# Kernel tuning notes

Measured on AMD Instinct MI355X. Metric: run time of the kernel, lower is better.

## Reference

```python
import jax, jax.numpy as jnp
import numpy as np

B, L, E, H, V, ENC = 64, 51, 512, 512, 30000, 2048


def setup_inputs() -> dict:
    key = jax.random.key(0)
    ks = jax.random.split(key, 12)
    encoder_out = jax.random.normal(ks[0], (B, ENC), jnp.float32)
    encoded_captions = jax.random.randint(ks[1], (B, L), 0, V)
    lengths = jax.random.randint(ks[2], (B,), 2, L + 1)
    lengths = lengths.at[0].set(L)  # ensure max(decode_lengths) == L-1 so T is static
    caption_lengths = lengths[:, None]

    def lin(k, out_d, in_d):
        bnd = 1.0 / np.sqrt(in_d)
        kw, kb = jax.random.split(k)
        w = jax.random.uniform(kw, (out_d, in_d), jnp.float32, -bnd, bnd)
        b = jax.random.uniform(kb, (out_d,), jnp.float32, -bnd, bnd)
        return w, b

    embedding_weight = jax.random.uniform(ks[3], (V, E), jnp.float32, -0.1, 0.1)
    w_ih, b_ih = lin(ks[4], 4 * H, E)
    w_hh, b_hh = lin(ks[5], 4 * H, H)
    w_init_h, b_init_h = lin(ks[6], H, ENC)
    w_init_c, b_init_c = lin(ks[7], H, ENC)
    w_fc = jax.random.uniform(ks[8], (V, H), jnp.float32, -0.1, 0.1)
    b_fc = jnp.zeros((V,), jnp.float32)
    return dict(encoder_out=encoder_out, encoded_captions=encoded_captions,
                caption_lengths=caption_lengths, embedding_weight=embedding_weight,
                w_ih=w_ih, b_ih=b_ih, w_hh=w_hh, b_hh=b_hh,
                w_init_h=w_init_h, b_init_h=b_init_h,
                w_init_c=w_init_c, b_init_c=b_init_c, w_fc=w_fc, b_fc=b_fc)


def _forward(encoder_out, embedding_weight, w_ih, b_ih, w_hh, b_hh,
             w_init_h, b_init_h, w_init_c, b_init_c, w_fc, b_fc,
             encoded_captions, caption_lengths):
    lengths = caption_lengths[:, 0]
    sort_ind = jnp.argsort(-lengths)          # descending-length sort
    enc = encoder_out[sort_ind]
    caps = encoded_captions[sort_ind]
    dec_len = lengths[sort_ind] - 1           # [B]
    embs = embedding_weight[caps]             # [B, L, E]
    h0 = enc @ w_init_h.T + b_init_h          # [B, H]
    c0 = enc @ w_init_c.T + b_init_c
    T = caps.shape[1] - 1                     # static max(decode_lengths)
    xs = (jnp.transpose(embs[:, :T], (1, 0, 2)), jnp.arange(T))

    # Note: the torch loop trims h,c to batch_size_t; because lengths are
    # sorted descending, trimmed rows never produce outputs again, so running
    # the full batch and masking finished rows yields identical predictions.
    def step(carry, xt):
        h, c = carry
        x, t = xt
        gates = x @ w_ih.T + b_ih + h @ w_hh.T + b_hh   # [B, 4H]
        i, f, g, o = jnp.split(gates, 4, axis=-1)       # LSTMCell gate order
        c = jax.nn.sigmoid(f) * c + jax.nn.sigmoid(i) * jnp.tanh(g)
        h = jax.nn.sigmoid(o) * jnp.tanh(c)
        preds = h @ w_fc.T + b_fc                        # dropout = identity (eval)
        preds = jnp.where((t < dec_len)[:, None], preds, 0.0)
        return (h, c), preds

    _, preds = jax.lax.scan(step, (h0, c0), xs)          # [T, B, V]
    predictions = jnp.transpose(preds, (1, 0, 2))        # [B, T, V]
    return predictions, caps, dec_len, sort_ind


def reference(encoder_out, encoded_captions, caption_lengths, embedding_weight,
              w_ih, b_ih, w_hh, b_hh, w_init_h, b_init_h, w_init_c, b_init_c,
              w_fc, b_fc):
    return _forward(encoder_out, embedding_weight, w_ih, b_ih, w_hh, b_hh,
                    w_init_h, b_init_h, w_init_c, b_init_c, w_fc, b_fc,
                    encoded_captions, caption_lengths)
```

## Files before the change

kernel.cpp:

```cpp
#include <hip/hip_runtime.h>

#define NB    64
#define LCAP  51
#define TT    50
#define HID   512
#define EMB   512
#define VOC   30000
#define ENCD  2048
#define G4    2048

typedef unsigned short u16;
typedef unsigned int   u32;
typedef __attribute__((ext_vector_type(8))) short bf16x8;
typedef __attribute__((ext_vector_type(4))) float f32x4;
typedef __attribute__((ext_vector_type(4))) unsigned int u32x4;

__device__ __forceinline__ u16 f2bf(float x) {
  union { float f; unsigned u; } v; v.f = x;
  unsigned r = v.u + 0x7fffu + ((v.u >> 16) & 1u);
  return (u16)(r >> 16);
}

__device__ __forceinline__ float fast_sigmoid(float x) {
  return 1.f / (1.f + __expf(-x));
}
__device__ __forceinline__ float fast_tanh(float x) {
  float xx = fminf(fmaxf(x, -10.f), 10.f);
  float e = __expf(2.f * xx);
  return (e - 1.f) * __frcp_rn(e + 1.f);
}

template <int SLEEP>
__device__ __forceinline__ void poll_flags16(const int* flg, int lane, u32 tt) {
  if (lane < 16) {
    const u32* myp = (const u32*)flg + lane;
    u32 f;
    for (;;) {
      asm volatile("global_load_dword %0, %1, off sc0 sc1"
                   : "=v"(f) : "v"(myp) : "memory");
      asm volatile("s_waitcnt vmcnt(0)" : "+v"(f) :: "memory");
      if (((f & 0xffu) >= tt) & (((f >> 8) & 0xffu) >= tt) &
          (((f >> 16) & 0xffu) >= tt) & ((f >> 24) >= tt)) break;
      __builtin_amdgcn_s_sleep(SLEEP);
    }
  }
}

__global__ __launch_bounds__(256) void sort_k(const int* __restrict__ cap_len,
                                              const int* __restrict__ caps,
                                              float* __restrict__ out,
                                              int* __restrict__ sind,
                                              int* __restrict__ dlen,
                                              int* __restrict__ trow,
                                              int* __restrict__ zmap,
                                              int* __restrict__ nact,
                                              int* __restrict__ flags,
                                              int* __restrict__ tileneed) {
  __shared__ int smlen[NB];
  __shared__ int smpos[NB];
  __shared__ int sdl[NB];
  __shared__ int cnt_s[TT];
  __shared__ int toff_s[TT];
  __shared__ int trow_s[NB * TT];
  int tid = threadIdx.x;
  if (tid < NB) { smlen[tid] = cap_len[tid]; flags[tid] = 0; }
  __syncthreads();
  if (tid < NB) {
    int li = smlen[tid];
    int rank = 0;
    for (int j = 0; j < NB; ++j) {
      int lj = smlen[j];
      rank += (lj > li || (lj == li && j < tid)) ? 1 : 0;
    }
    smpos[rank] = tid;
  }
  __syncthreads();
  if (tid < NB) {
    int src = smpos[tid];
    int dl = smlen[src] - 1;
    sind[tid] = src;
    dlen[tid] = dl;
    sdl[tid] = dl;
    float* caps_out = out + (size_t)NB * TT * VOC;
    for (int l = 0; l < LCAP; ++l)
      caps_out[tid * LCAP + l] = (float)caps[src * LCAP + l];
    out[96003264 + tid] = (float)dl;
    out[96003328 + tid] = (float)src;
  }
  __syncthreads();
  if (tid < TT) {
    int c = 0;
    for (int b = 0; b < NB; ++b) c += (sdl[b] > tid) ? 1 : 0;
    cnt_s[tid] = c;
  }
  __syncthreads();
  if (tid == 0) {
    int s = 0;
    for (int t = 0; t < TT; ++t) { toff_s[t] = s; s += cnt_s[t]; }
    *nact = s;
  }
  __syncthreads();
  if (tid < TT) {
    int t = tid;
    int o = toff_s[t];
    int z = t * NB - o;
    int c = cnt_s[t];
    for (int b = 0; b < NB; ++b) {
      int m = b * TT + t;
      if (b < c) trow_s[o + b] = m;
      else       zmap[z + (b - c)] = m;
    }
  }
  __syncthreads();
  int na = toff_s[TT - 1] + cnt_s[TT - 1];
  for (int k = tid; k < na; k += 256) trow[k] = trow_s[k];
  if (tid < 25) {
    int i = tid;
    if (i * 128 < na) {
      int k = min(i * 128 + 127, na - 1);
      tileneed[i] = (trow_s[k] % TT) + 2;
    }
  }
}

__global__ __launch_bounds__(256) void prep_k(const float* __restrict__ w_ih,
                                              const float* __restrict__ wh,
                                              const float* __restrict__ wc,
                                              const float* __restrict__ enc,
                                              const float* __restrict__ emb,
                                              const float* __restrict__ w_fc,
                                              const int* __restrict__ caps,
                                              const int* __restrict__ sind,
                                              u16* __restrict__ Wih,
                                              u16* __restrict__ Winit,
                                              u16* __restrict__ Ebf,
                                              u16* __restrict__ Xb,
                                              u16* __restrict__ Wfc) {
  int i = blockIdx.x * 256 + threadIdx.x;
  const float* src;
  u16* dstp;
  if (i < 262144) {
    src = w_ih + (size_t)i * 4;
    dstp = Wih + (size_t)i * 4;
  } else if (i < 786432) {
    int e = (i - 262144) * 4;
    int row = e >> 11, col = e & 2047;
    src = (row < 512) ? (wh + (size_t)row * 2048 + col)
                      : (wc + (size_t)(row - 512) * 2048 + col);
    dstp = Winit + (size_t)(i - 262144) * 4;
  } else if (i < 819200) {
    int e = (i - 786432) * 4;
    int r = e >> 11, k = e & 2047;
    src = enc + (size_t)sind[r] * ENCD + k;
    dstp = Ebf + (size_t)(i - 786432) * 4;
  } else if (i < 1228800) {
    int e = (i - 819200) * 4;
    int m = e >> 9, k = e & 511;
    unsigned b = ((unsigned)m * 5243u) >> 18;
    int t = m - (int)b * TT;
    int cap = caps[sind[b] * LCAP + t];
    src = emb + (size_t)cap * EMB + k;
    dstp = Xb + (size_t)(i - 819200) * 4;
  } else if (i < 5068800) {
    size_t idx = (size_t)(i - 1228800) * 4;
    src = w_fc + idx;
    dstp = Wfc + idx;
  } else return;
  float4 v = *(const float4*)src;
  ushort4 o;
  o.x = f2bf(v.x); o.y = f2bf(v.y); o.z = f2bf(v.z); o.w = f2bf(v.w);
  *(ushort4*)dstp = o;
}

#define BM 128
#define BN 128
#define BK 32
#define LDT 40

template <int EPI>
__global__ __launch_bounds__(256) void gemm_bt(const u16* __restrict__ A,
                                               const u16* __restrict__ Bm,
                                               int Mr, int Nr, int K,
                                               void* __restrict__ outv,
                                               float* __restrict__ out1,
                                               const float* __restrict__ bias0,
                                               const float* __restrict__ bias1) {
  __shared__ u16 As[BM * LDT];
  __shared__ u16 Bs[BN * LDT];
  int tid = threadIdx.x;
  int mBase = blockIdx.x * BM;
  int nBase = blockIdx.y * BN;

  int wid = tid >> 6, lane = tid & 63;
  int wm = (wid >> 1) * 64, wn = (wid & 1) * 64;
  int lm = lane & 15, lq = lane >> 4;

  f32x4 acc[4][4];
  for (int i = 0; i < 4; ++i)
    for (int j = 0; j < 4; ++j)
      acc[i][j] = (f32x4){0.f, 0.f, 0.f, 0.f};

  int nkt = K / BK;
  for (int kt = 0; kt < nkt; ++kt) {
    for (int it = 0; it < 2; ++it) {
      int li = tid + it * 256;
      int row = li >> 2, kq = li & 3;
      {
        int gr = min(mBase + row, Mr - 1);
        uint4 v = *(const uint4*)(A + (size_t)gr * K + kt * BK + kq * 8);
        *(uint4*)&As[row * LDT + kq * 8] = v;
      }
      {
        int gr = min(nBase + row, Nr - 1);
        uint4 v = *(const uint4*)(Bm + (size_t)gr * K + kt * BK + kq * 8);
        *(uint4*)&Bs[row * LDT + kq * 8] = v;
      }
    }
    __syncthreads();
    bf16x8 af[4], bfr[4];
    for (int i = 0; i < 4; ++i)
      af[i] = *(const bf16x8*)&As[(wm + i * 16 + lm) * LDT + lq * 8];
    for (int j = 0; j < 4; ++j)
      bfr[j] = *(const bf16x8*)&Bs[(wn + j * 16 + lm) * LDT + lq * 8];
    for (int i = 0; i < 4; ++i)
      for (int j = 0; j < 4; ++j)
        acc[i][j] = __builtin_amdgcn_mfma_f32_16x16x32_bf16(af[i], bfr[j], acc[i][j], 0, 0, 0);
    __syncthreads();
  }

  for (int i = 0; i < 4; ++i) {
    int rloc0 = wm + i * 16 + (lane >> 4) * 4;
    for (int j = 0; j < 4; ++j) {
      int col = nBase + wn + j * 16 + (lane & 15);
      for (int r = 0; r < 4; ++r) {
        int rloc = rloc0 + r;
        float v = acc[i][j][r];
        if (EPI == 0) {
          int row = mBase + rloc;
          if (row < Mr && col < Nr)
            ((float*)outv)[(size_t)row * Nr + col] = v + bias0[col] + bias1[col];
        } else {
          int row = mBase + rloc;
          if (row < Mr && col < Nr) {
            if (col < 512) {
              int jj = col >> 3;
              ((u16*)outv)[(size_t)jj * 512 + row * 8 + (col & 7)] = f2bf(v + bias0[col]);
            } else {
              out1[(size_t)row * 512 + (col - 512)] = v + bias1[col - 512];
            }
          }
        }
      }
    }
  }
}

__global__ __launch_bounds__(256, 1) void lstm_fc(const float* __restrict__ w_hh,
                                                  const float* __restrict__ xW,
                                                  const float* __restrict__ cbuf,
                                                  u32* __restrict__ hx,
                                                  u32* __restrict__ Hs32,
                                                  int* __restrict__ flg,
                                                  const u16* __restrict__ Wfc,
                                                  const float* __restrict__ b_fc,
                                                  const int* __restrict__ trow,
                                                  const int* __restrict__ zmap,
                                                  const int* __restrict__ nactp,
                                                  const int* __restrict__ tileneed,
                                                  float* __restrict__ out) {
  __shared__ __align__(16) char smem[43520];
  int tid = threadIdx.x;
  int wave = tid >> 6, lane = tid & 63;
  int lm = lane & 15, lq = lane >> 4;

  if (blockIdx.x < 64) {
    u16* wsm = (u16*)smem;
    float* gsmf = (float*)(smem + 33280);
    u32* hsh = (u32*)(smem + 33280 + 9216);
#define GSM(rr, cc) gsmf[(rr) * 36 + (cc)]
    int j = blockIdx.x;
    int u0 = j * 8;

    {
      int r = tid >> 3;
      int cc = (tid & 7) * 64;
      const float* src = w_hh + (size_t)((r >> 3) * HID + u0 + (r & 7)) * HID + cc;
      u16* dst = &wsm[r * 520 + cc];
#pragma unroll
      for (int q = 0; q < 16; ++q) {
        float4 v = ((const float4*)src)[q];
        ushort4 o; o.x = f2bf(v.x); o.y = f2bf(v.y); o.z = f2bf(v.z); o.w = f2bf(v.w);
        ((ushort4*)dst)[q] = o;
      }
    }
    __syncthreads();

    bf16x8 bfrag[2][16];
#pragma unroll
    for (int n = 0; n < 2; ++n)
#pragma unroll
      for (int kq = 0; kq < 16; ++kq)
        bfrag[n][kq] = *(const bf16x8*)&wsm[(n * 16 + lm) * 520 + kq * 32 + lq * 8];

    int b = tid >> 2, up = tid & 3;
    float creg[2];
    {
      float2 c2 = *(const float2*)&cbuf[(size_t)b * HID + u0 + 2 * up];
      creg[0] = c2.x; creg[1] = c2.y;
    }

    const int abase = lq * 256 + (wave * 16 + lm) * 4;

    for (int t = 0; t < TT; ++t) {
      const u32* hcur = hx + (size_t)(t & 1) * (NB * 256);
      u32* hnxt = hx + (size_t)((t + 1) & 1) * (NB * 256);

      float xg[4][2];
      {
        const float* xwp = xW + (size_t)(b * TT + t) * G4 + u0 + 2 * up;
#pragma unroll
        for (int g = 0; g < 4; ++g) {
          float2 v = *(const float2*)&xwp[g * HID];
          xg[g][0] = v.x; xg[g][1] = v.y;
        }
      }

      if (t > 0) {
        if (wave == 0) poll_flags16<1>(flg, lane, (u32)t);
        __syncthreads();
      }

      u32x4 raw[16];
#pragma unroll
      for (int kq = 0; kq < 16; ++kq) {
        const u32* p = hcur + abase + kq * 1024;
        asm volatile("global_load_dwordx4 %0, %1, off sc0 sc1"
                     : "=v"(raw[kq]) : "v"(p) : "memory");
      }
      asm volatile("s_waitcnt vmcnt(0)"
                   : "+v"(raw[0]), "+v"(raw[1]), "+v"(raw[2]), "+v"(raw[3]),
                     "+v"(raw[4]), "+v"(raw[5]), "+v"(raw[6]), "+v"(raw[7]),
                     "+v"(raw[8]), "+v"(raw[9]), "+v"(raw[10]), "+v"(raw[11]),
                     "+v"(raw[12]), "+v"(raw[13]), "+v"(raw[14]), "+v"(raw[15])
                   :: "memory");

      f32x4 acc0 = (f32x4){0.f, 0.f, 0.f, 0.f};
      f32x4 acc1 = (f32x4){0.f, 0.f, 0.f, 0.f};
#pragma unroll
      for (int kq = 0; kq < 16; ++kq) {
        bf16x8 a = __builtin_bit_cast(bf16x8, raw[kq]);
        acc0 = __builtin_amdgcn_mfma_f32_16x16x32_bf16(a, bfrag[0][kq], acc0, 0, 0, 0);
        acc1 = __builtin_amdgcn_mfma_f32_16x16x32_bf16(a, bfrag[1][kq], acc1, 0, 0, 0);
      }
#pragma unroll
      for (int r = 0; r < 4; ++r) {
        GSM(wave * 16 + lq * 4 + r, lm)      = acc0[r];
        GSM(wave * 16 + lq * 4 + r, 16 + lm) = acc1[r];
      }

      float hn2[2];
#pragma unroll
      for (int e = 0; e < 2; ++e) {
        int ul = 2 * up + e;
        float gi = GSM(b, ul)      + xg[0][e];
        float gf = GSM(b, 8 + ul)  + xg[1][e];
        float gg = GSM(b, 16 + ul) + xg[2][e];
        float go = GSM(b, 24 + ul) + xg[3][e];
        float cn = fast_sigmoid(gf) * creg[e] + fast_sigmoid(gi) * fast_tanh(gg);
        creg[e] = cn;
        hn2[e] = fast_sigmoid(go) * fast_tanh(cn);
      }
      hsh[b * 4 + up] = (u32)f2bf(hn2[0]) | ((u32)f2bf(hn2[1]) << 16);
      __syncthreads();

      if (tid < 64) {
        u32x4 hv = *(const u32x4*)&hsh[tid * 4];
        u32* dst = hnxt + j * 256 + tid * 4;
        asm volatile("global_store_dwordx4 %0, %1, off sc0 sc1"
                     :: "v"(dst), "v"(hv) : "memory");
        asm volatile("s_waitcnt vmcnt(0)" ::: "memory");
        if (tid == 0) {
          u32 fv = (u32)(t + 1);
          unsigned char* fj = (unsigned char*)flg + j;
          asm volatile("global_store_byte %0, %1, off sc0 sc1"
                       :: "v"(fj), "v"(fv) : "memory");
        }
        u32* hdst = Hs32 + (size_t)t * 16384 + j * 256 + tid * 4;
        asm volatile("global_store_dwordx4 %0, %1, off sc0 sc1"
                     :: "v"(hdst), "v"(hv) : "memory");
      }
    }
    if (wave == 0) {
      asm volatile("s_waitcnt vmcnt(0)" ::: "memory");
      if (lane == 0) {
        u32 fv = 51u;
        unsigned char* fj = (unsigned char*)flg + j;
        asm volatile("global_store_byte %0, %1, off sc0 sc1"
                     :: "v"(fj), "v"(fv) : "memory");
      }
    }
#undef GSM
  } else {
    u16* As = (u16*)smem;
    u16* Bs = (u16*)(smem + 10240);
    int* rmap_s = (int*)(smem + 20480);
    int* hsl_s = (int*)(smem + 20992);
    int* tn_s = (int*)(smem + 21504);
    const u16* HsU = (const u16*)Hs32;

    if (tid < 25) tn_s[tid] = tileneed[tid];
    int nactv = nactp[0];
    int ntiles = (nactv + 127) >> 7;
    int totjobs = ntiles * 235;
    __syncthreads();

    const int F = 192;
    int f = blockIdx.x - 64;
    int fs = (f & 7) * 24 + (f >> 3);
    int per = (totjobs + F - 1) / F;
    int J0 = fs * per;
    int J1 = min(J0 + per, totjobs);
    int wm = (wave >> 1) * 64, wn = (wave & 1) * 64;

    if (J0 < J1) {
      int p0 = J0 / ntiles, p1 = (J1 - 1) / ntiles;

      int lastNeed = 0;
      for (int rt = 0; rt < ntiles; ++rt) {
        int need = tn_s[rt];
        bool any = false;
        for (int p = p0; p <= p1; ++p) {
          int J = p * ntiles + rt;
          if (J >= J0 && J < J1) { any = true; break; }
        }
        if (!any) continue;
        if (need > lastNeed) {
          if (wave == 0) poll_flags16<64>(flg, lane, (u32)need);
          lastNeed = need;
        }
        __syncthreads();
        if (tid < 128) {
          int k = (rt << 7) + tid;
          int m = trow[(k < nactv) ? k : (nactv - 1)];
          int bb = (m * 5243) >> 18;
          int tt = m - bb * TT;
          rmap_s[tid] = m;
          hsl_s[tid] = tt * 32768 + bb * 8;
        }
        __syncthreads();

        for (int p = p0; p <= p1; ++p) {
          int J = p * ntiles + rt;
          if (J < J0 || J >= J1) continue;
          int nBase = p * 128;

          f32x4 acc[4][4];
          for (int i = 0; i < 4; ++i)
            for (int jj = 0; jj < 4; ++jj)
              acc[i][jj] = (f32x4){0.f, 0.f, 0.f, 0.f};

          for (int kt = 0; kt < 16; ++kt) {
            for (int it = 0; it < 2; ++it) {
              int li = tid + it * 256;
              int row = li >> 2, kq = li & 3;
              {
                uint4 v = *(const uint4*)(HsU + (size_t)hsl_s[row] + (kt * 4 + kq) * 512);
                *(uint4*)&As[row * LDT + kq * 8] = v;
              }
              {
                int gb = min(nBase + row, VOC - 1);
                uint4 v = *(const uint4*)(Wfc + (size_t)gb * 512 + kt * BK + kq * 8);
                *(uint4*)&Bs[row * LDT + kq * 8] = v;
              }
            }
            __syncthreads();
            bf16x8 af[4], bfr[4];
            for (int i = 0; i < 4; ++i)
              af[i] = *(const bf16x8*)&As[(wm + i * 16 + lm) * LDT + lq * 8];
            for (int jj = 0; jj < 4; ++jj)
              bfr[jj] = *(const bf16x8*)&Bs[(wn + jj * 16 + lm) * LDT + lq * 8];
            for (int i = 0; i < 4; ++i)
              for (int jj = 0; jj < 4; ++jj)
                acc[i][jj] = __builtin_amdgcn_mfma_f32_16x16x32_bf16(af[i], bfr[jj], acc[i][jj], 0, 0, 0);
            __syncthreads();
          }

          for (int i = 0; i < 4; ++i) {
            int rloc0 = wm + i * 16 + lq * 4;
            for (int jj = 0; jj < 4; ++jj) {
              int col = nBase + wn + jj * 16 + lm;
              if (col < VOC) {
                float bias = b_fc[col];
                for (int r = 0; r < 4; ++r) {
                  int m = rmap_s[rloc0 + r];
                  out[(size_t)m * VOC + col] = acc[i][jj][r] + bias;
                }
              }
            }
          }
        }
      }
    }

    int nz = NB * TT - nactv;
    float4 zz = {0.f, 0.f, 0.f, 0.f};
    for (int r = f; r < nz; r += F) {
      float4* dst = (float4*)(out + (size_t)zmap[r] * VOC);
      for (int c4 = tid; c4 < VOC / 4; c4 += 256) dst[c4] = zz;
    }
  }
}

extern "C" void kernel_launch(void* const* d_in, const int* in_sizes, int n_in,
                              void* d_out, int out_size, void* d_ws, size_t ws_size,
                              hipStream_t stream) {
  const float* encoder_out = (const float*)d_in[0];
  const int*   caps        = (const int*)d_in[1];
  const int*   cap_len     = (const int*)d_in[2];
  const float* emb         = (const float*)d_in[3];
  const float* w_ih        = (const float*)d_in[4];
  const float* b_ih        = (const float*)d_in[5];
  const float* w_hh        = (const float*)d_in[6];
  const float* b_hh        = (const float*)d_in[7];
  const float* w_init_h    = (const float*)d_in[8];
  const float* b_init_h    = (const float*)d_in[9];
  const float* w_init_c    = (const float*)d_in[10];
  const float* b_init_c    = (const float*)d_in[11];
  const float* w_fc        = (const float*)d_in[12];
  const float* b_fc        = (const float*)d_in[13];
  float* out = (float*)d_out;

  char* ws = (char*)d_ws;
  int*   sind    = (int*)(ws + 0);
  int*   dlen    = (int*)(ws + 256);
  int*   nact    = (int*)(ws + 512);
  int*   flags   = (int*)(ws + 576);
  int*   tilend  = (int*)(ws + 640);
  int*   trow    = (int*)(ws + 832);
  int*   zmap    = (int*)(ws + 13632);
  float* cbuf    = (float*)(ws + 26496);
  u16*   hbuf    = (u16*)(ws + 157568);
  float* xW      = (float*)(ws + 288640);
  u16*   Hs      = (u16*)(ws + 26503040);
  u16*   Xb      = (u16*)(ws + 29779840);
  u16*   Wih     = (u16*)(ws + 33056640);
  u16*   Winit   = (u16*)(ws + 35153792);
  u16*   Wfc     = (u16*)(ws + 39348096);
  u16*   Ebf     = (u16*)(ws + 70068096);

  sort_k<<<1, 256, 0, stream>>>(cap_len, caps, out, sind, dlen, trow, zmap,
                                nact, flags, tilend);
  prep_k<<<19800, 256, 0, stream>>>(w_ih, w_init_h, w_init_c, encoder_out,
                                    emb, w_fc, caps, sind,
                                    Wih, Winit, Ebf, Xb, Wfc);

  gemm_bt<1><<<dim3(1, 8), 256, 0, stream>>>(Ebf, Winit, 64, 1024, 2048,
                                             hbuf, cbuf, b_init_h, b_init_c);
  gemm_bt<0><<<dim3(25, 16), 256, 0, stream>>>(Xb, Wih, 3200, 2048, 512,
                                               xW, nullptr, b_ih, b_hh);
  lstm_fc<<<256, 256, 0, stream>>>(w_hh, xW, cbuf, (u32*)hbuf, (u32*)Hs, flags,
                                   Wfc, b_fc, trow, zmap, nact, tilend, out);
}
```

Baseline: 901.7 us.

## Fuse init h/c GEMM into LSTM kernel and reschedule FC job distribution

```diff
diff --git a/kernel.cpp b/kernel.cpp
--- a/kernel.cpp
+++ b/kernel.cpp
@@ -118,21 +118,18 @@
     int i = tid;
     if (i * 128 < na) {
       int k = min(i * 128 + 127, na - 1);
-      tileneed[i] = (trow_s[k] % TT) + 2;
+      tileneed[i] = (trow_s[k] % TT) + 3;
     }
   }
 }
 
 __global__ __launch_bounds__(256) void prep_k(const float* __restrict__ w_ih,
-                                              const float* __restrict__ wh,
-                                              const float* __restrict__ wc,
                                               const float* __restrict__ enc,
                                               const float* __restrict__ emb,
                                               const float* __restrict__ w_fc,
                                               const int* __restrict__ caps,
                                               const int* __restrict__ sind,
                                               u16* __restrict__ Wih,
-                                              u16* __restrict__ Winit,
                                               u16* __restrict__ Ebf,
                                               u16* __restrict__ Xb,
                                               u16* __restrict__ Wfc) {
@@ -142,27 +139,21 @@
   if (i < 262144) {
     src = w_ih + (size_t)i * 4;
     dstp = Wih + (size_t)i * 4;
-  } else if (i < 786432) {
+  } else if (i < 294912) {
     int e = (i - 262144) * 4;
-    int row = e >> 11, col = e & 2047;
-    src = (row < 512) ? (wh + (size_t)row * 2048 + col)
-                      : (wc + (size_t)(row - 512) * 2048 + col);
-    dstp = Winit + (size_t)(i - 262144) * 4;
-  } else if (i < 819200) {
-    int e = (i - 786432) * 4;
     int r = e >> 11, k = e & 2047;
     src = enc + (size_t)sind[r] * ENCD + k;
-    dstp = Ebf + (size_t)(i - 786432) * 4;
-  } else if (i < 1228800) {
-    int e = (i - 819200) * 4;
+    dstp = Ebf + (size_t)(i - 262144) * 4;
+  } else if (i < 704512) {
+    int e = (i - 294912) * 4;
     int m = e >> 9, k = e & 511;
     unsigned b = ((unsigned)m * 5243u) >> 18;
     int t = m - (int)b * TT;
     int cap = caps[sind[b] * LCAP + t];
     src = emb + (size_t)cap * EMB + k;
-    dstp = Xb + (size_t)(i - 819200) * 4;
-  } else if (i < 5068800) {
-    size_t idx = (size_t)(i - 1228800) * 4;
+    dstp = Xb + (size_t)(i - 294912) * 4;
+  } else if (i < 4544512) {
+    size_t idx = (size_t)(i - 704512) * 4;
     src = w_fc + idx;
     dstp = Wfc + idx;
   } else return;
@@ -177,12 +168,10 @@
 #define BK 32
 #define LDT 40
 
-template <int EPI>
 __global__ __launch_bounds__(256) void gemm_bt(const u16* __restrict__ A,
                                                const u16* __restrict__ Bm,
                                                int Mr, int Nr, int K,
-                                               void* __restrict__ outv,
-                                               float* __restrict__ out1,
+                                               float* __restrict__ outv,
                                                const float* __restrict__ bias0,
                                                const float* __restrict__ bias1) {
   __shared__ u16 As[BM * LDT];
@@ -233,31 +222,21 @@
     for (int j = 0; j < 4; ++j) {
       int col = nBase + wn + j * 16 + (lane & 15);
       for (int r = 0; r < 4; ++r) {
-        int rloc = rloc0 + r;
-        float v = acc[i][j][r];
-        if (EPI == 0) {
-          int row = mBase + rloc;
-          if (row < Mr && col < Nr)
-            ((float*)outv)[(size_t)row * Nr + col] = v + bias0[col] + bias1[col];
-        } else {
-          int row = mBase + rloc;
-          if (row < Mr && col < Nr) {
-            if (col < 512) {
-              int jj = col >> 3;
-              ((u16*)outv)[(size_t)jj * 512 + row * 8 + (col & 7)] = f2bf(v + bias0[col]);
-            } else {
-              out1[(size_t)row * 512 + (col - 512)] = v + bias1[col - 512];
-            }
-          }
-        }
+        int row = mBase + rloc0 + r;
+        if (row < Mr && col < Nr)
+          outv[(size_t)row * Nr + col] = acc[i][j][r] + bias0[col] + bias1[col];
       }
     }
   }
 }
 
 __global__ __launch_bounds__(256, 1) void lstm_fc(const float* __restrict__ w_hh,
+                                                  const float* __restrict__ w_init_h,
+                                                  const float* __restrict__ w_init_c,
+                                                  const float* __restrict__ b_init_h,
+                                                  const float* __restrict__ b_init_c,
+                                                  const u16* __restrict__ Ebf,
                                                   const float* __restrict__ xW,
-                                                  const float* __restrict__ cbuf,
                                                   u32* __restrict__ hx,
                                                   u32* __restrict__ Hs32,
                                                   int* __restrict__ flg,
@@ -304,9 +283,47 @@
 
     int b = tid >> 2, up = tid & 3;
     float creg[2];
+
     {
-      float2 c2 = *(const float2*)&cbuf[(size_t)b * HID + u0 + 2 * up];
-      creg[0] = c2.x; creg[1] = c2.y;
+      f32x4 iacc = (f32x4){0.f, 0.f, 0.f, 0.f};
+      const u16* aptr = Ebf + (size_t)(wave * 16 + lm) * 2048;
+      const float* wsrc = (lm < 8) ? (w_init_h + (size_t)(u0 + lm) * 2048)
+                                   : (w_init_c + (size_t)(u0 + (lm - 8)) * 2048);
+#pragma unroll 4
+      for (int kt = 0; kt < 64; ++kt) {
+        int ko = kt * 32 + lq * 8;
+        bf16x8 a = *(const bf16x8*)(aptr + ko);
+        float4 b0 = *(const float4*)(wsrc + ko);
+        float4 b1 = *(const float4*)(wsrc + ko + 4);
+        bf16x8 bfv;
+        bfv[0] = (short)f2bf(b0.x); bfv[1] = (short)f2bf(b0.y);
+        bfv[2] = (short)f2bf(b0.z); bfv[3] = (short)f2bf(b0.w);
+        bfv[4] = (short)f2bf(b1.x); bfv[5] = (short)f2bf(b1.y);
+        bfv[6] = (short)f2bf(b1.z); bfv[7] = (short)f2bf(b1.w);
+        iacc = __builtin_amdgcn_mfma_f32_16x16x32_bf16(a, bfv, iacc, 0, 0, 0);
+      }
+      float ibias = (lm < 8) ? b_init_h[u0 + lm] : b_init_c[u0 + (lm - 8)];
+#pragma unroll
+      for (int r = 0; r < 4; ++r)
+        GSM(wave * 16 + lq * 4 + r, lm) = iacc[r] + ibias;
+      creg[0] = GSM(b, 8 + 2 * up);
+      creg[1] = GSM(b, 8 + 2 * up + 1);
+      float h00 = GSM(b, 2 * up), h01 = GSM(b, 2 * up + 1);
+      hsh[b * 4 + up] = (u32)f2bf(h00) | ((u32)f2bf(h01) << 16);
+      __syncthreads();
+      if (tid < 64) {
+        u32x4 hv = *(const u32x4*)&hsh[tid * 4];
+        u32* dst = hx + j * 256 + tid * 4;
+        asm volatile("global_store_dwordx4 %0, %1, off sc0 sc1"
+                     :: "v"(dst), "v"(hv) : "memory");
+        asm volatile("s_waitcnt vmcnt(0)" ::: "memory");
+        if (tid == 0) {
+          u32 fv = 1u;
+          unsigned char* fj = (unsigned char*)flg + j;
+          asm volatile("global_store_byte %0, %1, off sc0 sc1"
+                       :: "v"(fj), "v"(fv) : "memory");
+        }
+      }
     }
 
     const int abase = lq * 256 + (wave * 16 + lm) * 4;
@@ -325,10 +342,8 @@
         }
       }
 
-      if (t > 0) {
-        if (wave == 0) poll_flags16<1>(flg, lane, (u32)t);
-        __syncthreads();
-      }
+      if (wave == 0) poll_flags16<1>(flg, lane, (u32)(t + 1));
+      __syncthreads();
 
       u32x4 raw[16];
 #pragma unroll
@@ -380,12 +395,12 @@
                      :: "v"(dst), "v"(hv) : "memory");
         asm volatile("s_waitcnt vmcnt(0)" ::: "memory");
         if (tid == 0) {
-          u32 fv = (u32)(t + 1);
+          u32 fv = (u32)(t + 2);
           unsigned char* fj = (unsigned char*)flg + j;
           asm volatile("global_store_byte %0, %1, off sc0 sc1"
                        :: "v"(fj), "v"(fv) : "memory");
         }
-        u32* hdst = Hs32 + (size_t)t * 16384 + j * 256 + tid * 4;
+        u32* hdst = Hs32 + ((size_t)tid * TT + t) * 256 + j * 4;
         asm volatile("global_store_dwordx4 %0, %1, off sc0 sc1"
                      :: "v"(hdst), "v"(hv) : "memory");
       }
@@ -393,7 +408,7 @@
     if (wave == 0) {
       asm volatile("s_waitcnt vmcnt(0)" ::: "memory");
       if (lane == 0) {
-        u32 fv = 51u;
+        u32 fv = 52u;
         unsigned char* fj = (unsigned char*)flg + j;
         asm volatile("global_store_byte %0, %1, off sc0 sc1"
                      :: "v"(fj), "v"(fv) : "memory");
@@ -404,9 +419,8 @@
     u16* As = (u16*)smem;
     u16* Bs = (u16*)(smem + 10240);
     int* rmap_s = (int*)(smem + 20480);
-    int* hsl_s = (int*)(smem + 20992);
-    int* tn_s = (int*)(smem + 21504);
-    const u16* HsU = (const u16*)Hs32;
+    int* tn_s = (int*)(smem + 20992);
+    const u16* HsA = (const u16*)Hs32;
 
     if (tid < 25) tn_s[tid] = tileneed[tid];
     int nactv = nactp[0];
@@ -416,86 +430,66 @@
 
     const int F = 192;
     int f = blockIdx.x - 64;
-    int fs = (f & 7) * 24 + (f >> 3);
-    int per = (totjobs + F - 1) / F;
-    int J0 = fs * per;
-    int J1 = min(J0 + per, totjobs);
     int wm = (wave >> 1) * 64, wn = (wave & 1) * 64;
 
-    if (J0 < J1) {
-      int p0 = J0 / ntiles, p1 = (J1 - 1) / ntiles;
-
-      int lastNeed = 0;
-      for (int rt = 0; rt < ntiles; ++rt) {
-        int need = tn_s[rt];
-        bool any = false;
-        for (int p = p0; p <= p1; ++p) {
-          int J = p * ntiles + rt;
-          if (J >= J0 && J < J1) { any = true; break; }
-        }
-        if (!any) continue;
-        if (need > lastNeed) {
-          if (wave == 0) poll_flags16<64>(flg, lane, (u32)need);
-          lastNeed = need;
+    int lastNeed = 0;
+    for (int job = f; job < totjobs; job += F) {
+      int rt = job / 235;
+      int nb = job - rt * 235;
+      int nBase = nb * 128;
+      int need = tn_s[rt];
+      if (need > lastNeed) {
+        if (wave == 0) poll_flags16<64>(flg, lane, (u32)need);
+        lastNeed = need;
+      }
+      __syncthreads();
+      if (tid < 128) {
+        int k = (rt << 7) + tid;
+        rmap_s[tid] = trow[(k < nactv) ? k : (nactv - 1)];
+      }
+      __syncthreads();
+
+      f32x4 acc[4][4];
+      for (int i = 0; i < 4; ++i)
+        for (int jj = 0; jj < 4; ++jj)
+          acc[i][jj] = (f32x4){0.f, 0.f, 0.f, 0.f};
+
+      for (int kt = 0; kt < 16; ++kt) {
+        for (int it = 0; it < 2; ++it) {
+          int li = tid + it * 256;
+          int row = li >> 2, kq = li & 3;
+          {
+            int gr = rmap_s[row];
+            uint4 v = *(const uint4*)(HsA + (size_t)gr * 512 + kt * BK + kq * 8);
+            *(uint4*)&As[row * LDT + kq * 8] = v;
+          }
+          {
+            int gb = min(nBase + row, VOC - 1);
+            uint4 v = *(const uint4*)(Wfc + (size_t)gb * 512 + kt * BK + kq * 8);
+            *(uint4*)&Bs[row * LDT + kq * 8] = v;
+          }
         }
         __syncthreads();
-        if (tid < 128) {
-          int k = (rt << 7) + tid;
-          int m = trow[(k < nactv) ? k : (nactv - 1)];
-          int bb = (m * 5243) >> 18;
-          int tt = m - bb * TT;
-          rmap_s[tid] = m;
-          hsl_s[tid] = tt * 32768 + bb * 8;
-        }
+        bf16x8 af[4], bfr[4];
+        for (int i = 0; i < 4; ++i)
+          af[i] = *(const bf16x8*)&As[(wm + i * 16 + lm) * LDT + lq * 8];
+        for (int jj = 0; jj < 4; ++jj)
+          bfr[jj] = *(const bf16x8*)&Bs[(wn + jj * 16 + lm) * LDT + lq * 8];
+        for (int i = 0; i < 4; ++i)
+          for (int jj = 0; jj < 4; ++jj)
+            acc[i][jj] = __builtin_amdgcn_mfma_f32_16x16x32_bf16(af[i], bfr[jj], acc[i][jj], 0, 0, 0);
         __syncthreads();
-
-        for (int p = p0; p <= p1; ++p) {
-          int J = p * ntiles + rt;
-          if (J < J0 || J >= J1) continue;
-          int nBase = p * 128;
-
-          f32x4 acc[4][4];
-          for (int i = 0; i < 4; ++i)
-            for (int jj = 0; jj < 4; ++jj)
-              acc[i][jj] = (f32x4){0.f, 0.f, 0.f, 0.f};
-
-          for (int kt = 0; kt < 16; ++kt) {
-            for (int it = 0; it < 2; ++it) {
-              int li = tid + it * 256;
-              int row = li >> 2, kq = li & 3;
-              {
-                uint4 v = *(const uint4*)(HsU + (size_t)hsl_s[row] + (kt * 4 + kq) * 512);
-                *(uint4*)&As[row * LDT + kq * 8] = v;
-              }
-              {
-                int gb = min(nBase + row, VOC - 1);
-                uint4 v = *(const uint4*)(Wfc + (size_t)gb * 512 + kt * BK + kq * 8);
-                *(uint4*)&Bs[row * LDT + kq * 8] = v;
-              }
-            }
-            __syncthreads();
-            bf16x8 af[4], bfr[4];
-            for (int i = 0; i < 4; ++i)
-              af[i] = *(const bf16x8*)&As[(wm + i * 16 + lm) * LDT + lq * 8];
-            for (int jj = 0; jj < 4; ++jj)
-              bfr[jj] = *(const bf16x8*)&Bs[(wn + jj * 16 + lm) * LDT + lq * 8];
-            for (int i = 0; i < 4; ++i)
-              for (int jj = 0; jj < 4; ++jj)
-                acc[i][jj] = __builtin_amdgcn_mfma_f32_16x16x32_bf16(af[i], bfr[jj], acc[i][jj], 0, 0, 0);
-            __syncthreads();
-          }
-
-          for (int i = 0; i < 4; ++i) {
-            int rloc0 = wm + i * 16 + lq * 4;
-            for (int jj = 0; jj < 4; ++jj) {
-              int col = nBase + wn + jj * 16 + lm;
-              if (col < VOC) {
-                float bias = b_fc[col];
-                for (int r = 0; r < 4; ++r) {
-                  int m = rmap_s[rloc0 + r];
-                  out[(size_t)m * VOC + col] = acc[i][jj][r] + bias;
-                }
-              }
+      }
+
+      for (int i = 0; i < 4; ++i) {
+        int rloc0 = wm + i * 16 + lq * 4;
+        for (int jj = 0; jj < 4; ++jj) {
+          int col = nBase + wn + jj * 16 + lm;
+          if (col < VOC) {
+            float bias = b_fc[col];
+            for (int r = 0; r < 4; ++r) {
+              int m = rmap_s[rloc0 + r];
+              out[(size_t)m * VOC + col] = acc[i][jj][r] + bias;
             }
           }
         }
@@ -538,26 +532,21 @@
   int*   tilend  = (int*)(ws + 640);
   int*   trow    = (int*)(ws + 832);
   int*   zmap    = (int*)(ws + 13632);
-  float* cbuf    = (float*)(ws + 26496);
   u16*   hbuf    = (u16*)(ws + 157568);
   float* xW      = (float*)(ws + 288640);
   u16*   Hs      = (u16*)(ws + 26503040);
   u16*   Xb      = (u16*)(ws + 29779840);
   u16*   Wih     = (u16*)(ws + 33056640);
-  u16*   Winit   = (u16*)(ws + 35153792);
   u16*   Wfc     = (u16*)(ws + 39348096);
   u16*   Ebf     = (u16*)(ws + 70068096);
 
   sort_k<<<1, 256, 0, stream>>>(cap_len, caps, out, sind, dlen, trow, zmap,
                                 nact, flags, tilend);
-  prep_k<<<19800, 256, 0, stream>>>(w_ih, w_init_h, w_init_c, encoder_out,
-                                    emb, w_fc, caps, sind,
-                                    Wih, Winit, Ebf, Xb, Wfc);
-
-  gemm_bt<1><<<dim3(1, 8), 256, 0, stream>>>(Ebf, Winit, 64, 1024, 2048,
-                                             hbuf, cbuf, b_init_h, b_init_c);
-  gemm_bt<0><<<dim3(25, 16), 256, 0, stream>>>(Xb, Wih, 3200, 2048, 512,
-                                               xW, nullptr, b_ih, b_hh);
-  lstm_fc<<<256, 256, 0, stream>>>(w_hh, xW, cbuf, (u32*)hbuf, (u32*)Hs, flags,
+  prep_k<<<17752, 256, 0, stream>>>(w_ih, encoder_out, emb, w_fc, caps, sind,
+                                    Wih, Ebf, Xb, Wfc);
+  gemm_bt<<<dim3(25, 16), 256, 0, stream>>>(Xb, Wih, 3200, 2048, 512,
+                                            xW, b_ih, b_hh);
+  lstm_fc<<<256, 256, 0, stream>>>(w_hh, w_init_h, w_init_c, b_init_h, b_init_c,
+                                   Ebf, xW, (u32*)hbuf, (u32*)Hs, flags,
                                    Wfc, b_fc, trow, zmap, nact, tilend, out);
 }
```

Result: faster. 808.0 us (-10.4%).
